# Kernel optimization log

Measured on AMD Instinct MI355X. Metric: run time of the kernel, lower is better.

## Reference

```python
import jax, jax.numpy as jnp
import numpy as np


def _warp_single(img, flow):
    """Bilinear warp of one image.
    img:  [H, W, C] float
    flow: [H, W, 2] float, flow[...,0]=dx (horizontal), flow[...,1]=dy (vertical)
    Samples img at (x + dx, y + dy) with zero padding outside the image.
    """
    H, W, _ = img.shape
    gx = jnp.arange(W, dtype=flow.dtype)[None, :] + flow[..., 0]  # [H, W]
    gy = jnp.arange(H, dtype=flow.dtype)[:, None] + flow[..., 1]  # [H, W]

    x0 = jnp.floor(gx)
    y0 = jnp.floor(gy)
    x1 = x0 + 1.0
    y1 = y0 + 1.0

    wx1 = gx - x0  # weight toward x1
    wy1 = gy - y0
    wx0 = 1.0 - wx1
    wy0 = 1.0 - wy1

    def gather(yi, xi):
        # valid mask before clipping; out-of-bounds contributes zero
        valid = (yi >= 0) & (yi < H) & (xi >= 0) & (xi < W)
        yc = jnp.clip(yi, 0, H - 1).astype(jnp.int32)
        xc = jnp.clip(xi, 0, W - 1).astype(jnp.int32)
        vals = img[yc, xc]  # [H, W, C] gather
        return vals * valid[..., None].astype(img.dtype)

    out = (gather(y0, x0) * (wy0 * wx0)[..., None]
           + gather(y0, x1) * (wy0 * wx1)[..., None]
           + gather(y1, x0) * (wy1 * wx0)[..., None]
           + gather(y1, x1) * (wy1 * wx1)[..., None])
    return out


def setup_inputs() -> dict:
    key = jax.random.key(0)
    k1, k2 = jax.random.split(key)
    N, H, W, C = 4, 1024, 1024, 8
    x = jax.random.normal(k1, (N, H, W, C), dtype=jnp.float32)
    u = jax.random.normal(k2, (N, H, W, 2), dtype=jnp.float32) * 4.0
    return {"x": x, "u": u}


def reference(x, u):
    # channel_last=True: x is NHWC. The original transposes to NCHW for the op
    # and back; the math is layout-independent, so we warp directly in NHWC.
    return jax.vmap(_warp_single)(x, u)
```

## Files before the change

kernel.cpp:

```cpp
#include <hip/hip_runtime.h>


typedef float vf2 __attribute__((ext_vector_type(2)));
typedef float vf4 __attribute__((ext_vector_type(4)));

__global__ __launch_bounds__(256) void Warp_41446434406635_kernel(
    const float* __restrict__ img,
    const float* __restrict__ flow,
    float* __restrict__ out)
{
    const int W = 1024, H = 1024;

    int tid = blockIdx.x * 256 + threadIdx.x;
    int g   = tid >> 1;
    int h   = tid & 1;

    int chunk  = g >> 5;
    int lane32 = g & 31;
    int pA = (chunk << 6) + lane32;
    int pB = pA + 32;

    vf2 fA = __builtin_nontemporal_load(reinterpret_cast<const vf2*>(flow) + pA);
    vf2 fB = __builtin_nontemporal_load(reinterpret_cast<const vf2*>(flow) + pB);

    int xA = pA & (W - 1), yA = (pA >> 10) & (H - 1), nA = pA >> 20;
    int xB = xA + 32;

    float gxA = (float)xA + fA.x, gyA = (float)yA + fA.y;
    float x0fA = floorf(gxA), y0fA = floorf(gyA);
    int ix0A = (int)x0fA, iy0A = (int)y0fA;
    int ix1A = ix0A + 1,  iy1A = iy0A + 1;
    float wx1A = gxA - x0fA, wy1A = gyA - y0fA;
    float wx0A = 1.0f - wx1A, wy0A = 1.0f - wy1A;
    bool vx0A = (ix0A >= 0) & (ix0A < W);
    bool vx1A = (ix1A >= 0) & (ix1A < W);
    bool vy0A = (iy0A >= 0) & (iy0A < H);
    bool vy1A = (iy1A >= 0) & (iy1A < H);
    float w00A = (vy0A & vx0A) ? wy0A * wx0A : 0.0f;
    float w01A = (vy0A & vx1A) ? wy0A * wx1A : 0.0f;
    float w10A = (vy1A & vx0A) ? wy1A * wx0A : 0.0f;
    float w11A = (vy1A & vx1A) ? wy1A * wx1A : 0.0f;
    int cx0A = min(max(ix0A, 0), W - 1);
    int cx1A = min(max(ix1A, 0), W - 1);
    int cy0A = min(max(iy0A, 0), H - 1);
    int cy1A = min(max(iy1A, 0), H - 1);

    float gxB = (float)xB + fB.x, gyB = (float)yA + fB.y;
    float x0fB = floorf(gxB), y0fB = floorf(gyB);
    int ix0B = (int)x0fB, iy0B = (int)y0fB;
    int ix1B = ix0B + 1,  iy1B = iy0B + 1;
    float wx1B = gxB - x0fB, wy1B = gyB - y0fB;
    float wx0B = 1.0f - wx1B, wy0B = 1.0f - wy1B;
    bool vx0B = (ix0B >= 0) & (ix0B < W);
    bool vx1B = (ix1B >= 0) & (ix1B < W);
    bool vy0B = (iy0B >= 0) & (iy0B < H);
    bool vy1B = (iy1B >= 0) & (iy1B < H);
    float w00B = (vy0B & vx0B) ? wy0B * wx0B : 0.0f;
    float w01B = (vy0B & vx1B) ? wy0B * wx1B : 0.0f;
    float w10B = (vy1B & vx0B) ? wy1B * wx0B : 0.0f;
    float w11B = (vy1B & vx1B) ? wy1B * wx1B : 0.0f;
    int cx0B = min(max(ix0B, 0), W - 1);
    int cx1B = min(max(ix1B, 0), W - 1);
    int cy0B = min(max(iy0B, 0), H - 1);
    int cy1B = min(max(iy1B, 0), H - 1);

    const float* base = img + ((size_t)nA << 23) + (h << 2);

    vf4 a00 = *reinterpret_cast<const vf4*>(base + ((size_t)cy0A << 13) + (cx0A << 3));
    vf4 a01 = *reinterpret_cast<const vf4*>(base + ((size_t)cy0A << 13) + (cx1A << 3));
    vf4 a10 = *reinterpret_cast<const vf4*>(base + ((size_t)cy1A << 13) + (cx0A << 3));
    vf4 a11 = *reinterpret_cast<const vf4*>(base + ((size_t)cy1A << 13) + (cx1A << 3));
    vf4 b00 = *reinterpret_cast<const vf4*>(base + ((size_t)cy0B << 13) + (cx0B << 3));
    vf4 b01 = *reinterpret_cast<const vf4*>(base + ((size_t)cy0B << 13) + (cx1B << 3));
    vf4 b10 = *reinterpret_cast<const vf4*>(base + ((size_t)cy1B << 13) + (cx0B << 3));
    vf4 b11 = *reinterpret_cast<const vf4*>(base + ((size_t)cy1B << 13) + (cx1B << 3));

    vf4 oA, oB;
    oA.x = fmaf(w00A, a00.x, fmaf(w01A, a01.x, fmaf(w10A, a10.x, w11A * a11.x)));
    oA.y = fmaf(w00A, a00.y, fmaf(w01A, a01.y, fmaf(w10A, a10.y, w11A * a11.y)));
    oA.z = fmaf(w00A, a00.z, fmaf(w01A, a01.z, fmaf(w10A, a10.z, w11A * a11.z)));
    oA.w = fmaf(w00A, a00.w, fmaf(w01A, a01.w, fmaf(w10A, a10.w, w11A * a11.w)));
    oB.x = fmaf(w00B, b00.x, fmaf(w01B, b01.x, fmaf(w10B, b10.x, w11B * b11.x)));
    oB.y = fmaf(w00B, b00.y, fmaf(w01B, b01.y, fmaf(w10B, b10.y, w11B * b11.y)));
    oB.z = fmaf(w00B, b00.z, fmaf(w01B, b01.z, fmaf(w10B, b10.z, w11B * b11.z)));
    oB.w = fmaf(w00B, b00.w, fmaf(w01B, b01.w, fmaf(w10B, b10.w, w11B * b11.w)));

    vf4* o4 = reinterpret_cast<vf4*>(out);
    __builtin_nontemporal_store(oA, o4 + ((size_t)pA << 1) + h);
    __builtin_nontemporal_store(oB, o4 + ((size_t)pB << 1) + h);

    (void)H;
}

extern "C" void kernel_launch(void* const* d_in, const int* in_sizes, int n_in,
                              void* d_out, int out_size, void* d_ws, size_t ws_size,
                              hipStream_t stream) {
    const float* x = (const float*)d_in[0];
    const float* u = (const float*)d_in[1];
    float* out = (float*)d_out;

    Warp_41446434406635_kernel<<<16384, 256, 0, stream>>>(x, u, out);
}
```

Before: 76.02 us.

## Split each pixel across four lanes and combine x-corners with a warp shuffle

The work mapping changes from one thread handling two pixels, half the channels each, to four threads per pixel. Each thread owns one x-corner and one channel half, loads two rows, and adds the x-neighbour's partial sum with __shfl_xor. This raises the number of threads and loads in flight and lowers registers per thread, at the cost of four times more threads. It also adds a redundant flow load and index computation in each lane, plus shuffle overhead, and half the lanes sit idle during the store.

```diff
diff --git a/kernel.cpp b/kernel.cpp
--- a/kernel.cpp
+++ b/kernel.cpp
@@ -12,82 +12,51 @@
     const int W = 1024, H = 1024;
 
     int tid = blockIdx.x * 256 + threadIdx.x;
-    int g   = tid >> 1;
-    int h   = tid & 1;
+    int p = tid >> 2;
+    int r = tid & 3;
 
-    int chunk  = g >> 5;
-    int lane32 = g & 31;
-    int pA = (chunk << 6) + lane32;
-    int pB = pA + 32;
+    vf2 f = __builtin_nontemporal_load(reinterpret_cast<const vf2*>(flow) + p);
 
-    vf2 fA = __builtin_nontemporal_load(reinterpret_cast<const vf2*>(flow) + pA);
-    vf2 fB = __builtin_nontemporal_load(reinterpret_cast<const vf2*>(flow) + pB);
+    int x = p & (W - 1), y = (p >> 10) & (H - 1), n = p >> 20;
 
-    int xA = pA & (W - 1), yA = (pA >> 10) & (H - 1), nA = pA >> 20;
-    int xB = xA + 32;
+    float gx = (float)x + f.x, gy = (float)y + f.y;
+    float x0f = floorf(gx), y0f = floorf(gy);
+    int ix0 = (int)x0f, iy0 = (int)y0f;
+    int iy1 = iy0 + 1;
+    float wx1 = gx - x0f, wy1 = gy - y0f;
 
-    float gxA = (float)xA + fA.x, gyA = (float)yA + fA.y;
-    float x0fA = floorf(gxA), y0fA = floorf(gyA);
-    int ix0A = (int)x0fA, iy0A = (int)y0fA;
-    int ix1A = ix0A + 1,  iy1A = iy0A + 1;
-    float wx1A = gxA - x0fA, wy1A = gyA - y0fA;
-    float wx0A = 1.0f - wx1A, wy0A = 1.0f - wy1A;
-    bool vx0A = (ix0A >= 0) & (ix0A < W);
-    bool vx1A = (ix1A >= 0) & (ix1A < W);
-    bool vy0A = (iy0A >= 0) & (iy0A < H);
-    bool vy1A = (iy1A >= 0) & (iy1A < H);
-    float w00A = (vy0A & vx0A) ? wy0A * wx0A : 0.0f;
-    float w01A = (vy0A & vx1A) ? wy0A * wx1A : 0.0f;
-    float w10A = (vy1A & vx0A) ? wy1A * wx0A : 0.0f;
-    float w11A = (vy1A & vx1A) ? wy1A * wx1A : 0.0f;
-    int cx0A = min(max(ix0A, 0), W - 1);
-    int cx1A = min(max(ix1A, 0), W - 1);
-    int cy0A = min(max(iy0A, 0), H - 1);
-    int cy1A = min(max(iy1A, 0), H - 1);
+    int xr = ix0 + (r >> 1);
+    float wxl = (r >> 1) ? wx1 : (1.0f - wx1);
+    if ((xr < 0) | (xr >= W)) wxl = 0.0f;
+    float wy0v = ((iy0 >= 0) & (iy0 < H)) ? (1.0f - wy1) : 0.0f;
+    float wy1v = ((iy1 >= 0) & (iy1 < H)) ? wy1 : 0.0f;
+    float w0 = wy0v * wxl;
+    float w1 = wy1v * wxl;
 
-    float gxB = (float)xB + fB.x, gyB = (float)yA + fB.y;
-    float x0fB = floorf(gxB), y0fB = floorf(gyB);
-    int ix0B = (int)x0fB, iy0B = (int)y0fB;
-    int ix1B = ix0B + 1,  iy1B = iy0B + 1;
-    float wx1B = gxB - x0fB, wy1B = gyB - y0fB;
-    float wx0B = 1.0f - wx1B, wy0B = 1.0f - wy1B;
-    bool vx0B = (ix0B >= 0) & (ix0B < W);
-    bool vx1B = (ix1B >= 0) & (ix1B < W);
-    bool vy0B = (iy0B >= 0) & (iy0B < H);
-    bool vy1B = (iy1B >= 0) & (iy1B < H);
-    float w00B = (vy0B & vx0B) ? wy0B * wx0B : 0.0f;
-    float w01B = (vy0B & vx1B) ? wy0B * wx1B : 0.0f;
-    float w10B = (vy1B & vx0B) ? wy1B * wx0B : 0.0f;
-    float w11B = (vy1B & vx1B) ? wy1B * wx1B : 0.0f;
-    int cx0B = min(max(ix0B, 0), W - 1);
-    int cx1B = min(max(ix1B, 0), W - 1);
-    int cy0B = min(max(iy0B, 0), H - 1);
-    int cy1B = min(max(iy1B, 0), H - 1);
+    int cx  = min(max(xr, 0), W - 1);
+    int cy0 = min(max(iy0, 0), H - 1);
+    int cy1 = min(max(iy1, 0), H - 1);
 
-    const float* base = img + ((size_t)nA << 23) + (h << 2);
+    const float* base = img + ((size_t)n << 23) + (cx << 3) + ((r & 1) << 2);
+    vf4 v0 = *reinterpret_cast<const vf4*>(base + ((size_t)cy0 << 13));
+    vf4 v1 = *reinterpret_cast<const vf4*>(base + ((size_t)cy1 << 13));
 
-    vf4 a00 = *reinterpret_cast<const vf4*>(base + ((size_t)cy0A << 13) + (cx0A << 3));
-    vf4 a01 = *reinterpret_cast<const vf4*>(base + ((size_t)cy0A << 13) + (cx1A << 3));
-    vf4 a10 = *reinterpret_cast<const vf4*>(base + ((size_t)cy1A << 13) + (cx0A << 3));
-    vf4 a11 = *reinterpret_cast<const vf4*>(base + ((size_t)cy1A << 13) + (cx1A << 3));
-    vf4 b00 = *reinterpret_cast<const vf4*>(base + ((size_t)cy0B << 13) + (cx0B << 3));
-    vf4 b01 = *reinterpret_cast<const vf4*>(base + ((size_t)cy0B << 13) + (cx1B << 3));
-    vf4 b10 = *reinterpret_cast<const vf4*>(base + ((size_t)cy1B << 13) + (cx0B << 3));
-    vf4 b11 = *reinterpret_cast<const vf4*>(base + ((size_t)cy1B << 13) + (cx1B << 3));
+    vf4 s;
+    s.x = fmaf(w0, v0.x, w1 * v1.x);
+    s.y = fmaf(w0, v0.y, w1 * v1.y);
+    s.z = fmaf(w0, v0.z, w1 * v1.z);
+    s.w = fmaf(w0, v0.w, w1 * v1.w);
 
-    vf4 oA, oB;
-    oA.x = fmaf(w00A, a00.x, fmaf(w01A, a01.x, fmaf(w10A, a10.x, w11A * a11.x)));
-    oA.y = fmaf(w00A, a00.y, fmaf(w01A, a01.y, fmaf(w10A, a10.y, w11A * a11.y)));
-    oA.z = fmaf(w00A, a00.z, fmaf(w01A, a01.z, fmaf(w10A, a10.z, w11A * a11.z)));
-    oA.w = fmaf(w00A, a00.w, fmaf(w01A, a01.w, fmaf(w10A, a10.w, w11A * a11.w)));
-    oB.x = fmaf(w00B, b00.x, fmaf(w01B, b01.x, fmaf(w10B, b10.x, w11B * b11.x)));
-    oB.y = fmaf(w00B, b00.y, fmaf(w01B, b01.y, fmaf(w10B, b10.y, w11B * b11.y)));
-    oB.z = fmaf(w00B, b00.z, fmaf(w01B, b01.z, fmaf(w10B, b10.z, w11B * b11.z)));
-    oB.w = fmaf(w00B, b00.w, fmaf(w01B, b01.w, fmaf(w10B, b10.w, w11B * b11.w)));
+    vf4 o;
+    o.x = s.x + __shfl_xor(s.x, 2);
+    o.y = s.y + __shfl_xor(s.y, 2);
+    o.z = s.z + __shfl_xor(s.z, 2);
+    o.w = s.w + __shfl_xor(s.w, 2);
 
-    vf4* o4 = reinterpret_cast<vf4*>(out);
-    __builtin_nontemporal_store(oA, o4 + ((size_t)pA << 1) + h);
-    __builtin_nontemporal_store(oB, o4 + ((size_t)pB << 1) + h);
+    if (r < 2) {
+        vf4* o4 = reinterpret_cast<vf4*>(out);
+        __builtin_nontemporal_store(o, o4 + ((size_t)p << 1) + (r & 1));
+    }
 
     (void)H;
 }
@@ -99,5 +68,5 @@
     const float* u = (const float*)d_in[1];
     float* out = (float*)d_out;
 
-    Warp_41446434406635_kernel<<<16384, 256, 0, stream>>>(x, u, out);
+    Warp_41446434406635_kernel<<<65536, 256, 0, stream>>>(x, u, out);
 }
```

Result: slower. 82.16 us (+8.1%).
